# Optimization experiments

Hardware: AMD Instinct MI355X
Metric: run time of the kernel (lower is better)

## Reference

```python
import jax, jax.numpy as jnp
import numpy as np

B, T, D, F, E, K = 2, 2048, 1024, 4096, 8, 2

def setup_inputs() -> dict:
    key = jax.random.key(0)
    k0, k1, k2, k3 = jax.random.split(key, 4)
    return {
        "x": jax.random.normal(k0, (B, T, D), jnp.float32),
        "Wg": jax.random.normal(k1, (D, E), jnp.float32) * (D ** -0.5),
        "W1": jax.random.normal(k2, (E, D, F), jnp.float32) * (D ** -0.5),
        "b1": jnp.zeros((E, F), jnp.float32),
        "W2": jax.random.normal(k3, (E, F, D), jnp.float32) * (F ** -0.5),
        "b2": jnp.zeros((E, D), jnp.float32),
        "topk": K,
    }

def reference(x, Wg, W1, b1, W2, b2, topk):
    n_experts = Wg.shape[-1]
    # Gating logits [B, T, E]
    gating = jnp.einsum('btd,de->bte', x, Wg)
    _, idx = jax.lax.top_k(gating, topk)
    # 0/1 mask of selected experts per token [B, T, E]
    mask = jax.nn.one_hot(idx, n_experts, dtype=x.dtype).sum(axis=-2)
    # Source does `gating -= 1/mask - 1`: no-op where mask==1, -inf where mask==0
    gate = jax.nn.softmax(jnp.where(mask > 0, gating, -jnp.inf), axis=-1)
    # Dense masked per-expert compute, exactly as the source (expert(x * mask_e))
    xm = x[:, :, None, :] * mask[:, :, :, None]          # [B, T, E, D]
    h = jax.nn.gelu(jnp.einsum('bted,edf->btef', xm, W1) + b1)  # [B, T, E, F]
    out_e = jnp.einsum('btef,efd->bted', h, W2) + b2     # [B, T, E, D]
    # Gate and sum over experts
    return jnp.sum(out_e * gate[..., None], axis=-2)      # [B, T, D]
```

## Files before the change

kernel.cpp:

```cpp
#include <hip/hip_runtime.h>
#include <hip/hip_bf16.h>
#include <math.h>

#define NB 2
#define NT 2048
#define NTOK 4096
#define DD 1024
#define FF 4096
#define NE 8
#define KSEL 2
#define BM 128
#define BN 128
#define BK 32
#define ROWCAP 9216
#define ROWTILES 72
#define KP2 2

typedef __attribute__((ext_vector_type(8))) short short8_t;
typedef __attribute__((ext_vector_type(4))) float f32x4;

__device__ __forceinline__ unsigned short f2bf(float f){
  unsigned u = __float_as_uint(f);
  unsigned r = (u + 0x7fffu + ((u >> 16) & 1u)) >> 16;
  return (unsigned short)r;
}

__device__ __forceinline__ int xcd_swz(int lin, int nwg){
  int q = nwg >> 3, r = nwg & 7;
  int xcd = lin & 7, idx = lin >> 3;
  return (xcd < r ? xcd * (q + 1) : r * (q + 1) + (xcd - r) * q) + idx;
}

#define GLOAD_LDS(g, l) \
  __builtin_amdgcn_global_load_lds((const __attribute__((address_space(1))) void*)(g), \
                                   (__attribute__((address_space(3))) void*)(l), 16, 0, 0)
#define VMCNT0 asm volatile("s_waitcnt vmcnt(0)" ::: "memory")
#define RAWBAR __builtin_amdgcn_s_barrier()


__global__ void k_prep_transpose(const float* __restrict__ x, const float* __restrict__ wg,
                                 short* __restrict__ xb, int* __restrict__ topk_idx,
                                 float* __restrict__ topk_gate, int* __restrict__ counts,
                                 const float* __restrict__ W1, const float* __restrict__ W2,
                                 short* __restrict__ w1t, short* __restrict__ w2t){
  __shared__ short T[64][134];
  if (blockIdx.x < 1024){
    int wid = threadIdx.x >> 6, lane = threadIdx.x & 63;
    int t = blockIdx.x * 4 + wid;
    const float* xr = x + (size_t)t * DD;
    short* xbr = xb + (size_t)t * DD;
    double acc[NE];
#pragma unroll
    for (int e = 0; e < NE; ++e) acc[e] = 0.0;
#pragma unroll
    for (int p = 0; p < 4; ++p){
      int d = p * 256 + lane * 4;
      float4 v = *(const float4*)(xr + d);
      short4 o;
      o.x = (short)f2bf(v.x); o.y = (short)f2bf(v.y);
      o.z = (short)f2bf(v.z); o.w = (short)f2bf(v.w);
      *(short4*)(xbr + d) = o;
      const float* w0 = wg + (size_t)d * NE;
      float vv[4] = {v.x, v.y, v.z, v.w};
#pragma unroll
      for (int j = 0; j < 4; ++j){
        double xv = (double)vv[j];
#pragma unroll
        for (int e = 0; e < NE; ++e) acc[e] += xv * (double)w0[j * NE + e];
      }
    }
#pragma unroll
    for (int e = 0; e < NE; ++e){
#pragma unroll
      for (int s = 32; s; s >>= 1) acc[e] += __shfl_xor(acc[e], s, 64);
    }
    if (lane == 0){
      int i0 = 0; double v0 = acc[0];
#pragma unroll
      for (int e = 1; e < NE; ++e) if (acc[e] > v0){ v0 = acc[e]; i0 = e; }
      int i1 = -1; double v1 = -1e300;
#pragma unroll
      for (int e = 0; e < NE; ++e) if (e != i0 && acc[e] > v1){ v1 = acc[e]; i1 = e; }
      double g0 = 1.0 / (1.0 + exp(v1 - v0));
      topk_idx[2 * t] = i0; topk_idx[2 * t + 1] = i1;
      topk_gate[2 * t] = (float)g0; topk_gate[2 * t + 1] = (float)(1.0 - g0);
      atomicAdd(&counts[i0], 1);
      atomicAdd(&counts[i1], 1);
    }
    return;
  }
  int id = blockIdx.x - 1024;
  bool isW2 = id >= 4096;
  int rem = id & 4095;
  int e = rem >> 9;
  int tr = rem & 511;
  int R, C, c0, r0;
  const float* in; short* out;
  if (!isW2){ R = DD; C = FF; c0 = (tr & 63) * 64; r0 = (tr >> 6) * 128;
              in = W1 + (size_t)e * R * C; out = w1t + (size_t)e * R * C; }
  else      { R = FF; C = DD; c0 = (tr & 15) * 64; r0 = (tr >> 4) * 128;
              in = W2 + (size_t)e * R * C; out = w2t + (size_t)e * R * C; }
  int t = threadIdx.x;
  int rr = t >> 4, c4 = (t & 15) * 4;
#pragma unroll
  for (int p = 0; p < 8; ++p){
    int row = p * 16 + rr;
    float4 v = *(const float4*)(in + (size_t)(r0 + row) * C + c0 + c4);
    T[c4 + 0][row] = (short)f2bf(v.x);
    T[c4 + 1][row] = (short)f2bf(v.y);
    T[c4 + 2][row] = (short)f2bf(v.z);
    T[c4 + 3][row] = (short)f2bf(v.w);
  }
  __syncthreads();
  int c8 = (t & 15) * 8;
#pragma unroll
  for (int q = 0; q < 4; ++q){
    int orow = q * 16 + rr;
    short4 lo = *(const short4*)&T[orow][c8];
    short4 hi = *(const short4*)&T[orow][c8 + 4];
    short8_t w;
    w[0] = lo.x; w[1] = lo.y; w[2] = lo.z; w[3] = lo.w;
    w[4] = hi.x; w[5] = hi.y; w[6] = hi.z; w[7] = hi.w;
    *(short8_t*)(out + (size_t)(c0 + orow) * R + r0 + c8) = w;
  }
}


__global__ void k_route_all(const int* __restrict__ counts, const int* __restrict__ topk_idx,
                            const float* __restrict__ topk_gate, int* __restrict__ poff_g,
                            int* __restrict__ row_token, float* __restrict__ row_gate,
                            int* __restrict__ slot_of){
  __shared__ int poff[NE + 1], cur[NE], rends[NE];
  if (threadIdx.x == 0){
    int off = 0;
    for (int e = 0; e < NE; ++e){
      poff[e] = off; cur[e] = off; rends[e] = off + counts[e];
      off += (counts[e] + BM - 1) & ~(BM - 1);
    }
    poff[NE] = off;
    for (int e = 0; e <= NE; ++e) poff_g[e] = poff[e];
  }
  __syncthreads();
  for (int t = threadIdx.x; t < NTOK; t += 256){
#pragma unroll
    for (int k = 0; k < KSEL; ++k){
      int e = topk_idx[2 * t + k];
      float g = topk_gate[2 * t + k];
      int slot = atomicAdd(&cur[e], 1);
      row_token[slot] = t;
      row_gate[slot] = g;
      slot_of[2 * t + k] = slot;
    }
  }
  __syncthreads();
#pragma unroll
  for (int e = 0; e < NE; ++e)
    for (int s = rends[e] + (int)threadIdx.x; s < poff[e + 1]; s += 256){
      row_token[s] = 0; row_gate[s] = 0.f;
    }
}


__launch_bounds__(256, 4)
__global__ void k_gemm1(const short* __restrict__ xb, const short* __restrict__ w1t,
                        const float* __restrict__ b1, short* __restrict__ h,
                        const int* __restrict__ row_token, const int* __restrict__ poff){
  __shared__ short As[2][BM * BK];
  __shared__ short Bs[2][BN * BK];
  int wg = xcd_swz(blockIdx.x, ROWTILES * (FF / BN));
  int g = wg >> 6, t6 = wg & 63;
  int bx = (g >> 2) * 8 + (t6 & 7);
  int by = (g & 3) * 8 + (t6 >> 3);
  int row0 = bx * BM;
  if (row0 >= poff[NE]) return;
  int e = 0;
  while (row0 >= poff[e + 1]) ++e;
  int n0 = by * BN;
  int tid = threadIdx.x;

  const short* asrc[2]; const short* bsrc[2];
#pragma unroll
  for (int p = 0; p < 2; ++p){
    int L = p * 256 + tid;
    int r = L >> 2, c = L & 3;
    int cd = c ^ ((r >> 1) & 3);
    int tok = row_token[row0 + r];
    asrc[p] = xb + (size_t)tok * DD + cd * 8;
    bsrc[p] = w1t + (size_t)e * FF * DD + (size_t)(n0 + r) * DD + cd * 8;
  }

  f32x4 acc[4][4];
#pragma unroll
  for (int i = 0; i < 4; ++i)
#pragma unroll
    for (int j = 0; j < 4; ++j) acc[i][j] = (f32x4){0.f, 0.f, 0.f, 0.f};

  int wid = tid >> 6, lane = tid & 63;
  int wr = wid >> 1, wc = wid & 1;
  int lrow = lane & 15, lk = lane >> 4;

  auto STAGE = [&](int nb, int k0){
#pragma unroll
    for (int p = 0; p < 2; ++p){
      GLOAD_LDS(asrc[p] + k0, &As[nb][0] + tid * 8 + p * 2048);
      GLOAD_LDS(bsrc[p] + k0, &Bs[nb][0] + tid * 8 + p * 2048);
    }
  };

  STAGE(0, 0);
  VMCNT0; RAWBAR;

  const int NKT = DD / BK;
#pragma unroll 1
  for (int kt = 0; kt < NKT; ++kt){
    int b = kt & 1;
    bool more = (kt + 1 < NKT);
    if (more) STAGE(b ^ 1, (kt + 1) * BK);
    short8_t a[4], bb[4];
#pragma unroll
    for (int m = 0; m < 4; ++m){
      int r = wr * 64 + m * 16 + lrow;
      a[m] = *(const short8_t*)(&As[b][0] + r * BK + ((lk ^ ((r >> 1) & 3)) * 8));
    }
#pragma unroll
    for (int n = 0; n < 4; ++n){
      int r = wc * 64 + n * 16 + lrow;
      bb[n] = *(const short8_t*)(&Bs[b][0] + r * BK + ((lk ^ ((r >> 1) & 3)) * 8));
    }
#pragma unroll
    for (int m = 0; m < 4; ++m)
#pragma unroll
      for (int n = 0; n < 4; ++n)
        acc[m][n] = __builtin_amdgcn_mfma_f32_16x16x32_bf16(a[m], bb[n], acc[m][n], 0, 0, 0);
    if (more) VMCNT0;
    RAWBAR;
  }

  const float* b1e = b1 + (size_t)e * FF;
  float bias[4];
#pragma unroll
  for (int n = 0; n < 4; ++n) bias[n] = b1e[n0 + wc * 64 + n * 16 + lrow];
#pragma unroll
  for (int m = 0; m < 4; ++m){
#pragma unroll
    for (int j = 0; j < 4; ++j){
      int row = row0 + wr * 64 + m * 16 + lk * 4 + j;
      short* hr = h + (size_t)row * FF + n0 + wc * 64 + lrow;
#pragma unroll
      for (int n = 0; n < 4; ++n){
        float v = acc[m][n][j] + bias[n];
        float u = 0.7978845608028654f * (v + 0.044715f * v * v * v);
        float gl = v / (1.0f + __expf(-2.0f * u));
        hr[n * 16] = (short)f2bf(gl);
      }
    }
  }
}


__launch_bounds__(256, 4)
__global__ void k_gemm2(const short* __restrict__ h, const short* __restrict__ w2t,
                        const float* __restrict__ b2, float* __restrict__ ya,
                        float* __restrict__ yb, const int* __restrict__ poff){
  __shared__ short As[2][BM * BK];
  __shared__ short Bs[2][BN * BK];
  int wg = xcd_swz(blockIdx.x, ROWTILES * (DD / BN) * KP2);
  int kz = wg / (ROWTILES * (DD / BN));
  int c5 = wg % (ROWTILES * (DD / BN));
  int g = c5 >> 5, t5 = c5 & 31;
  int bx = g * 4 + (t5 & 3);
  int by = t5 >> 2;
  int row0 = bx * BM;
  if (row0 >= poff[NE]) return;
  int e = 0;
  while (row0 >= poff[e + 1]) ++e;
  int n0 = by * BN;
  int tid = threadIdx.x;

  const short* asrc[2]; const short* bsrc[2];
#pragma unroll
  for (int p = 0; p < 2; ++p){
    int L = p * 256 + tid;
    int r = L >> 2, c = L & 3;
    int cd = c ^ ((r >> 1) & 3);
    asrc[p] = h + (size_t)(row0 + r) * FF + cd * 8;
    bsrc[p] = w2t + (size_t)e * DD * FF + (size_t)(n0 + r) * FF + cd * 8;
  }

  f32x4 acc[4][4];
#pragma unroll
  for (int i = 0; i < 4; ++i)
#pragma unroll
    for (int j = 0; j < 4; ++j) acc[i][j] = (f32x4){0.f, 0.f, 0.f, 0.f};

  int wid = tid >> 6, lane = tid & 63;
  int wr = wid >> 1, wc = wid & 1;
  int lrow = lane & 15, lk = lane >> 4;

  auto STAGE = [&](int nb, int k0){
#pragma unroll
    for (int p = 0; p < 2; ++p){
      GLOAD_LDS(asrc[p] + k0, &As[nb][0] + tid * 8 + p * 2048);
      GLOAD_LDS(bsrc[p] + k0, &Bs[nb][0] + tid * 8 + p * 2048);
    }
  };

  int kbeg = kz * (FF / KP2);
  STAGE(0, kbeg);
  VMCNT0; RAWBAR;

  const int NKT = (FF / KP2) / BK;
#pragma unroll 1
  for (int kt = 0; kt < NKT; ++kt){
    int b = kt & 1;
    bool more = (kt + 1 < NKT);
    if (more) STAGE(b ^ 1, kbeg + (kt + 1) * BK);
    short8_t a[4], bb[4];
#pragma unroll
    for (int m = 0; m < 4; ++m){
      int r = wr * 64 + m * 16 + lrow;
      a[m] = *(const short8_t*)(&As[b][0] + r * BK + ((lk ^ ((r >> 1) & 3)) * 8));
    }
#pragma unroll
    for (int n = 0; n < 4; ++n){
      int r = wc * 64 + n * 16 + lrow;
      bb[n] = *(const short8_t*)(&Bs[b][0] + r * BK + ((lk ^ ((r >> 1) & 3)) * 8));
    }
#pragma unroll
    for (int m = 0; m < 4; ++m)
#pragma unroll
      for (int n = 0; n < 4; ++n)
        acc[m][n] = __builtin_amdgcn_mfma_f32_16x16x32_bf16(a[m], bb[n], acc[m][n], 0, 0, 0);
    if (more) VMCNT0;
    RAWBAR;
  }

  float* y = (kz == 0) ? ya : yb;
  const float* b2e = b2 + (size_t)e * DD;
  float bias[4];
#pragma unroll
  for (int n = 0; n < 4; ++n) bias[n] = (kz == 0) ? b2e[n0 + wc * 64 + n * 16 + lrow] : 0.0f;
#pragma unroll
  for (int m = 0; m < 4; ++m){
#pragma unroll
    for (int j = 0; j < 4; ++j){
      int row = row0 + wr * 64 + m * 16 + lk * 4 + j;
      float* yr = y + (size_t)row * DD + n0 + wc * 64 + lrow;
#pragma unroll
      for (int n = 0; n < 4; ++n)
        yr[n * 16] = acc[m][n][j] + bias[n];
    }
  }
}


__global__ void k_combine(const float* __restrict__ ya, const float* __restrict__ yb,
                          const int* __restrict__ slot_of, const float* __restrict__ topk_gate,
                          float* __restrict__ out){
  int i = blockIdx.x * 256 + threadIdx.x;
  int t = i >> 8;
  int c4 = (i & 255) * 4;
  int s0 = slot_of[2 * t], s1 = slot_of[2 * t + 1];
  float g0 = topk_gate[2 * t], g1 = topk_gate[2 * t + 1];
  float4 a0 = *(const float4*)(ya + (size_t)s0 * DD + c4);
  float4 b0 = *(const float4*)(yb + (size_t)s0 * DD + c4);
  float4 a1 = *(const float4*)(ya + (size_t)s1 * DD + c4);
  float4 b1 = *(const float4*)(yb + (size_t)s1 * DD + c4);
  float4 o;
  o.x = g0 * (a0.x + b0.x) + g1 * (a1.x + b1.x);
  o.y = g0 * (a0.y + b0.y) + g1 * (a1.y + b1.y);
  o.z = g0 * (a0.z + b0.z) + g1 * (a1.z + b1.z);
  o.w = g0 * (a0.w + b0.w) + g1 * (a1.w + b1.w);
  *(float4*)(out + (size_t)t * DD + c4) = o;
}


extern "C" void kernel_launch(void* const* d_in, const int* in_sizes, int n_in,
                              void* d_out, int out_size, void* d_ws, size_t ws_size,
                              hipStream_t stream){
  (void)in_sizes; (void)n_in; (void)out_size; (void)ws_size;
  const float* x  = (const float*)d_in[0];
  const float* Wg = (const float*)d_in[1];
  const float* W1 = (const float*)d_in[2];
  const float* b1 = (const float*)d_in[3];
  const float* W2 = (const float*)d_in[4];
  const float* b2 = (const float*)d_in[5];
  float* out = (float*)d_out;
  char* ws = (char*)d_ws;

  int*   counts    = (int*)(ws + 0);
  int*   poff      = (int*)(ws + 256);
  int*   topk_idx  = (int*)(ws + 1024);
  float* topk_gate = (float*)(ws + 33792);
  int*   row_token = (int*)(ws + 66560);
  float* row_gate  = (float*)(ws + 103424);
  int*   slot_of   = (int*)(ws + 140288);
  short* xb        = (short*)(ws + 173056);
  short* w1t       = (short*)(ws + 8561664);
  short* w2t       = (short*)(ws + 75670528);
  short* h         = (short*)(ws + 142779392);
  float* ya        = (float*)(ws + 173056);
  float* yb        = (float*)(ws + 37921792);

  hipMemsetAsync(counts, 0, 32, stream);

  k_prep_transpose<<<dim3(1024 + 8192), 256, 0, stream>>>(x, Wg, xb, topk_idx, topk_gate,
                                                          counts, W1, W2, w1t, w2t);
  k_route_all<<<dim3(1), 256, 0, stream>>>(counts, topk_idx, topk_gate, poff,
                                           row_token, row_gate, slot_of);
  k_gemm1<<<dim3(ROWTILES * (FF / BN)), 256, 0, stream>>>(xb, w1t, b1, h, row_token, poff);
  k_gemm2<<<dim3(ROWTILES * (DD / BN) * KP2), 256, 0, stream>>>(h, w2t, b2, ya, yb, poff);
  k_combine<<<dim3(NTOK * DD / 4 / 256), 256, 0, stream>>>(ya, yb, slot_of, topk_gate, out);
}
```

Measured before the change: 412.7 us.

## Fuse gated combine into GEMM2 epilogue via float atomics into output

Removes the separate combine kernel and the two split-K partial buffers (ya/yb). GEMM2 now multiplies each row's result by its gate and atomically adds it into the zeroed output row of the original token, skipping padding rows whose gate is zero. This drops a full round trip of the partial results through memory and one kernel launch. In exchange it adds an output memset and many scalar fp32 atomics with contention (2 experts × 2 K-splits per element), and the summation order is no longer deterministic.

Result: slower. 446.7 us (+8.2%).

```diff
diff --git a/kernel.cpp b/kernel.cpp
--- a/kernel.cpp
+++ b/kernel.cpp
@@ -128,8 +128,7 @@
 
 __global__ void k_route_all(const int* __restrict__ counts, const int* __restrict__ topk_idx,
                             const float* __restrict__ topk_gate, int* __restrict__ poff_g,
-                            int* __restrict__ row_token, float* __restrict__ row_gate,
-                            int* __restrict__ slot_of){
+                            int* __restrict__ row_token, float* __restrict__ row_gate){
   __shared__ int poff[NE + 1], cur[NE], rends[NE];
   if (threadIdx.x == 0){
     int off = 0;
@@ -149,7 +148,6 @@
       int slot = atomicAdd(&cur[e], 1);
       row_token[slot] = t;
       row_gate[slot] = g;
-      slot_of[2 * t + k] = slot;
     }
   }
   __syncthreads();
@@ -260,8 +258,9 @@
 
 __launch_bounds__(256, 4)
 __global__ void k_gemm2(const short* __restrict__ h, const short* __restrict__ w2t,
-                        const float* __restrict__ b2, float* __restrict__ ya,
-                        float* __restrict__ yb, const int* __restrict__ poff){
+                        const float* __restrict__ b2, float* __restrict__ out,
+                        const int* __restrict__ row_token, const float* __restrict__ row_gate,
+                        const int* __restrict__ poff){
   __shared__ short As[2][BM * BK];
   __shared__ short Bs[2][BN * BK];
   int wg = xcd_swz(blockIdx.x, ROWTILES * (DD / BN) * KP2);
@@ -335,7 +334,6 @@
     RAWBAR;
   }
 
-  float* y = (kz == 0) ? ya : yb;
   const float* b2e = b2 + (size_t)e * DD;
   float bias[4];
 #pragma unroll
@@ -345,33 +343,16 @@
 #pragma unroll
     for (int j = 0; j < 4; ++j){
       int row = row0 + wr * 64 + m * 16 + lk * 4 + j;
-      float* yr = y + (size_t)row * DD + n0 + wc * 64 + lrow;
-#pragma unroll
-      for (int n = 0; n < 4; ++n)
-        yr[n * 16] = acc[m][n][j] + bias[n];
-    }
-  }
-}
-
-
-__global__ void k_combine(const float* __restrict__ ya, const float* __restrict__ yb,
-                          const int* __restrict__ slot_of, const float* __restrict__ topk_gate,
-                          float* __restrict__ out){
-  int i = blockIdx.x * 256 + threadIdx.x;
-  int t = i >> 8;
-  int c4 = (i & 255) * 4;
-  int s0 = slot_of[2 * t], s1 = slot_of[2 * t + 1];
-  float g0 = topk_gate[2 * t], g1 = topk_gate[2 * t + 1];
-  float4 a0 = *(const float4*)(ya + (size_t)s0 * DD + c4);
-  float4 b0 = *(const float4*)(yb + (size_t)s0 * DD + c4);
-  float4 a1 = *(const float4*)(ya + (size_t)s1 * DD + c4);
-  float4 b1 = *(const float4*)(yb + (size_t)s1 * DD + c4);
-  float4 o;
-  o.x = g0 * (a0.x + b0.x) + g1 * (a1.x + b1.x);
-  o.y = g0 * (a0.y + b0.y) + g1 * (a1.y + b1.y);
-  o.z = g0 * (a0.z + b0.z) + g1 * (a1.z + b1.z);
-  o.w = g0 * (a0.w + b0.w) + g1 * (a1.w + b1.w);
-  *(float4*)(out + (size_t)t * DD + c4) = o;
+      float gt = row_gate[row];
+      if (gt != 0.f){
+        int tok = row_token[row];
+        float* orow = out + (size_t)tok * DD + n0 + wc * 64 + lrow;
+#pragma unroll
+        for (int n = 0; n < 4; ++n)
+          atomicAdd(&orow[n * 16], gt * (acc[m][n][j] + bias[n]));
+      }
+    }
+  }
 }
 
 
@@ -394,21 +375,19 @@
   float* topk_gate = (float*)(ws + 33792);
   int*   row_token = (int*)(ws + 66560);
   float* row_gate  = (float*)(ws + 103424);
-  int*   slot_of   = (int*)(ws + 140288);
   short* xb        = (short*)(ws + 173056);
   short* w1t       = (short*)(ws + 8561664);
   short* w2t       = (short*)(ws + 75670528);
   short* h         = (short*)(ws + 142779392);
-  float* ya        = (float*)(ws + 173056);
-  float* yb        = (float*)(ws + 37921792);
 
   hipMemsetAsync(counts, 0, 32, stream);
+  hipMemsetAsync(out, 0, (size_t)NTOK * DD * sizeof(float), stream);
 
   k_prep_transpose<<<dim3(1024 + 8192), 256, 0, stream>>>(x, Wg, xb, topk_idx, topk_gate,
                                                           counts, W1, W2, w1t, w2t);
   k_route_all<<<dim3(1), 256, 0, stream>>>(counts, topk_idx, topk_gate, poff,
-                                           row_token, row_gate, slot_of);
+                                           row_token, row_gate);
   k_gemm1<<<dim3(ROWTILES * (FF / BN)), 256, 0, stream>>>(xb, w1t, b1, h, row_token, poff);
-  k_gemm2<<<dim3(ROWTILES * (DD / BN) * KP2), 256, 0, stream>>>(h, w2t, b2, ya, yb, poff);
-  k_combine<<<dim3(NTOK * DD / 4 / 256), 256, 0, stream>>>(ya, yb, slot_of, topk_gate, out);
-}
+  k_gemm2<<<dim3(ROWTILES * (DD / BN) * KP2), 256, 0, stream>>>(h, w2t, b2, out,
+                                                                row_token, row_gate, poff);
+}
```

## Move W2 transpose into the gemm1 launch to overlap with expert GEMM

Applied to the files above, without the earlier changes.

The W2 fp32-to-bf16 transpose blocks are taken out of the prep kernel and appended as extra workgroups in the gemm1 launch, which now shares one static LDS buffer between GEMM tiles and transpose tiles. Memory-bound transpose work can then fill CUs alongside or after the compute-bound GEMM tiles instead of delaying routing and gemm1. The cost is that the routing step no longer waits on the W2 transpose, and the combined kernel's launch bounds and LDS footprint now apply to the transpose blocks too, which may affect occupancy or tail behaviour.

After: 405.4 us, median of 2. About the same (-1.8%).

```diff
diff --git a/kernel.cpp b/kernel.cpp
--- a/kernel.cpp
+++ b/kernel.cpp
@@ -15,6 +15,7 @@
 #define ROWCAP 9216
 #define ROWTILES 72
 #define KP2 2
+#define NG1 (ROWTILES * (FF / BN))
 
 typedef __attribute__((ext_vector_type(8))) short short8_t;
 typedef __attribute__((ext_vector_type(4))) float f32x4;
@@ -37,12 +38,37 @@
 #define VMCNT0 asm volatile("s_waitcnt vmcnt(0)" ::: "memory")
 #define RAWBAR __builtin_amdgcn_s_barrier()
 
-
-__global__ void k_prep_transpose(const float* __restrict__ x, const float* __restrict__ wg,
-                                 short* __restrict__ xb, int* __restrict__ topk_idx,
-                                 float* __restrict__ topk_gate, int* __restrict__ counts,
-                                 const float* __restrict__ W1, const float* __restrict__ W2,
-                                 short* __restrict__ w1t, short* __restrict__ w2t){
+__device__ __forceinline__ void transpose_tile(const float* in, short* out, int R, int C,
+                                               int r0, int c0, short (*T)[134], int t){
+  int rr = t >> 4, c4 = (t & 15) * 4;
+#pragma unroll
+  for (int p = 0; p < 8; ++p){
+    int row = p * 16 + rr;
+    float4 v = *(const float4*)(in + (size_t)(r0 + row) * C + c0 + c4);
+    T[c4 + 0][row] = (short)f2bf(v.x);
+    T[c4 + 1][row] = (short)f2bf(v.y);
+    T[c4 + 2][row] = (short)f2bf(v.z);
+    T[c4 + 3][row] = (short)f2bf(v.w);
+  }
+  __syncthreads();
+  int c8 = (t & 15) * 8;
+#pragma unroll
+  for (int q = 0; q < 4; ++q){
+    int orow = q * 16 + rr;
+    short4 lo = *(const short4*)&T[orow][c8];
+    short4 hi = *(const short4*)&T[orow][c8 + 4];
+    short8_t w;
+    w[0] = lo.x; w[1] = lo.y; w[2] = lo.z; w[3] = lo.w;
+    w[4] = hi.x; w[5] = hi.y; w[6] = hi.z; w[7] = hi.w;
+    *(short8_t*)(out + (size_t)(c0 + orow) * R + r0 + c8) = w;
+  }
+}
+
+
+__global__ void k_prep_w1t(const float* __restrict__ x, const float* __restrict__ wg,
+                           short* __restrict__ xb, int* __restrict__ topk_idx,
+                           float* __restrict__ topk_gate, int* __restrict__ counts,
+                           const float* __restrict__ W1, short* __restrict__ w1t){
   __shared__ short T[64][134];
   if (blockIdx.x < 1024){
     int wid = threadIdx.x >> 6, lane = threadIdx.x & 63;
@@ -90,39 +116,10 @@
     return;
   }
   int id = blockIdx.x - 1024;
-  bool isW2 = id >= 4096;
-  int rem = id & 4095;
-  int e = rem >> 9;
-  int tr = rem & 511;
-  int R, C, c0, r0;
-  const float* in; short* out;
-  if (!isW2){ R = DD; C = FF; c0 = (tr & 63) * 64; r0 = (tr >> 6) * 128;
-              in = W1 + (size_t)e * R * C; out = w1t + (size_t)e * R * C; }
-  else      { R = FF; C = DD; c0 = (tr & 15) * 64; r0 = (tr >> 4) * 128;
-              in = W2 + (size_t)e * R * C; out = w2t + (size_t)e * R * C; }
-  int t = threadIdx.x;
-  int rr = t >> 4, c4 = (t & 15) * 4;
-#pragma unroll
-  for (int p = 0; p < 8; ++p){
-    int row = p * 16 + rr;
-    float4 v = *(const float4*)(in + (size_t)(r0 + row) * C + c0 + c4);
-    T[c4 + 0][row] = (short)f2bf(v.x);
-    T[c4 + 1][row] = (short)f2bf(v.y);
-    T[c4 + 2][row] = (short)f2bf(v.z);
-    T[c4 + 3][row] = (short)f2bf(v.w);
-  }
-  __syncthreads();
-  int c8 = (t & 15) * 8;
-#pragma unroll
-  for (int q = 0; q < 4; ++q){
-    int orow = q * 16 + rr;
-    short4 lo = *(const short4*)&T[orow][c8];
-    short4 hi = *(const short4*)&T[orow][c8 + 4];
-    short8_t w;
-    w[0] = lo.x; w[1] = lo.y; w[2] = lo.z; w[3] = lo.w;
-    w[4] = hi.x; w[5] = hi.y; w[6] = hi.z; w[7] = hi.w;
-    *(short8_t*)(out + (size_t)(c0 + orow) * R + r0 + c8) = w;
-  }
+  int e = id >> 9, tr = id & 511;
+  int c0 = (tr & 63) * 64, r0 = (tr >> 6) * 128;
+  transpose_tile(W1 + (size_t)e * DD * FF, w1t + (size_t)e * DD * FF, DD, FF, r0, c0, T,
+                 threadIdx.x);
 }
 
 
@@ -162,12 +159,22 @@
 
 
 __launch_bounds__(256, 4)
-__global__ void k_gemm1(const short* __restrict__ xb, const short* __restrict__ w1t,
-                        const float* __restrict__ b1, short* __restrict__ h,
-                        const int* __restrict__ row_token, const int* __restrict__ poff){
-  __shared__ short As[2][BM * BK];
-  __shared__ short Bs[2][BN * BK];
-  int wg = xcd_swz(blockIdx.x, ROWTILES * (FF / BN));
+__global__ void k_gemm1_w2t(const short* __restrict__ xb, const short* __restrict__ w1t,
+                            const float* __restrict__ b1, short* __restrict__ h,
+                            const int* __restrict__ row_token, const int* __restrict__ poff,
+                            const float* __restrict__ W2, short* __restrict__ w2t){
+  __shared__ short smem[16384];
+  if (blockIdx.x >= NG1){
+    int id = blockIdx.x - NG1;
+    int e = id >> 9, tr = id & 511;
+    int c0 = (tr & 15) * 64, r0 = (tr >> 4) * 128;
+    transpose_tile(W2 + (size_t)e * FF * DD, w2t + (size_t)e * FF * DD, FF, DD, r0, c0,
+                   (short (*)[134])smem, threadIdx.x);
+    return;
+  }
+  short (*As)[BM * BK] = (short (*)[BM * BK])smem;
+  short (*Bs)[BN * BK] = (short (*)[BN * BK])(smem + 8192);
+  int wg = xcd_swz(blockIdx.x, NG1);
   int g = wg >> 6, t6 = wg & 63;
   int bx = (g >> 2) * 8 + (t6 & 7);
   int by = (g & 3) * 8 + (t6 >> 3);
@@ -404,11 +411,12 @@
 
   hipMemsetAsync(counts, 0, 32, stream);
 
-  k_prep_transpose<<<dim3(1024 + 8192), 256, 0, stream>>>(x, Wg, xb, topk_idx, topk_gate,
-                                                          counts, W1, W2, w1t, w2t);
+  k_prep_w1t<<<dim3(1024 + 4096), 256, 0, stream>>>(x, Wg, xb, topk_idx, topk_gate,
+                                                    counts, W1, w1t);
   k_route_all<<<dim3(1), 256, 0, stream>>>(counts, topk_idx, topk_gate, poff,
                                            row_token, row_gate, slot_of);
-  k_gemm1<<<dim3(ROWTILES * (FF / BN)), 256, 0, stream>>>(xb, w1t, b1, h, row_token, poff);
+  k_gemm1_w2t<<<dim3(NG1 + 4096), 256, 0, stream>>>(xb, w1t, b1, h, row_token, poff,
+                                                    W2, w2t);
   k_gemm2<<<dim3(ROWTILES * (DD / BN) * KP2), 256, 0, stream>>>(h, w2t, b2, ya, yb, poff);
   k_combine<<<dim3(NTOK * DD / 4 / 256), 256, 0, stream>>>(ya, yb, slot_of, topk_gate, out);
 }
```
